# Kernel tuning notes

Hardware: AMD Instinct MI355X
Metric: run time of the kernel (lower is better)

Reference implementation:

```python
import jax, jax.numpy as jnp
import numpy as np

D_MODEL, D_STATE, D_CONV, EXPAND = 1024, 16, 4, 2
D_INNER = EXPAND * D_MODEL
BATCH, L = 2, 2048


def setup_inputs() -> dict:
    key = jax.random.key(0)
    ks = jax.random.split(key, 8)
    s = lambda fan: 1.0 / float(np.sqrt(fan))
    x = jax.random.normal(ks[0], (BATCH, L, D_MODEL), jnp.float32)
    W_in = jax.random.normal(ks[1], (D_MODEL, 2 * D_INNER), jnp.float32) * s(D_MODEL)
    conv_w = jax.random.normal(ks[2], (D_INNER, 1, D_CONV), jnp.float32) * s(D_CONV)
    conv_b = jax.random.normal(ks[3], (D_INNER,), jnp.float32) * 0.1
    W_x = jax.random.normal(ks[4], (D_INNER, 2 * D_STATE + 1), jnp.float32) * s(D_INNER)
    w_dt = jax.random.normal(ks[5], (D_INNER,), jnp.float32)
    b_dt = jax.random.normal(ks[6], (D_INNER,), jnp.float32) * 0.1
    W_out = jax.random.normal(ks[7], (D_INNER, D_MODEL), jnp.float32) * s(D_INNER)
    A_log = jnp.log(jnp.broadcast_to(jnp.arange(1, D_STATE + 1, dtype=jnp.float32), (D_INNER, D_STATE)))
    Dp = jnp.ones((D_INNER,), jnp.float32)
    return dict(x=x, W_in=W_in, conv_w=conv_w, conv_b=conv_b, W_x=W_x,
                w_dt=w_dt, b_dt=b_dt, A_log=A_log, Dp=Dp, W_out=W_out)


def _silu(v):
    return v * jax.nn.sigmoid(v)


def _forward(x, W_in, conv_w, conv_b, W_x, w_dt, b_dt, A_log, Dp, W_out):
    xz = x @ W_in                                   # (B,L,2*Di)
    x_, z = jnp.split(xz, 2, axis=-1)               # (B,L,Di) each
    # causal depthwise conv over length (== torch pad d_conv-1 both sides then [:L])
    xc = jnp.transpose(x_, (0, 2, 1))               # (B,Di,L)
    xc = jax.lax.conv_general_dilated(
        xc, conv_w, window_strides=(1,), padding=[(D_CONV - 1, 0)],
        dimension_numbers=('NCH', 'OIH', 'NCH'), feature_group_count=D_INNER)
    xc = xc + conv_b[None, :, None]
    x_ = _silu(jnp.transpose(xc, (0, 2, 1)))        # (B,L,Di)

    bcd = x_ @ W_x                                  # (B,L,2N+1)
    B_ = bcd[..., :D_STATE]                         # (B,L,N)
    C = bcd[..., D_STATE:2 * D_STATE]               # (B,L,N)
    dt = jax.nn.softplus(bcd[..., -1:] * w_dt + b_dt)  # (B,L,Di)
    A = -jnp.exp(A_log)                             # (Di,N)

    def step(h, inp):
        dt_t, B_t, C_t, x_t = inp                   # (B,Di),(B,N),(B,N),(B,Di)
        dA = jnp.exp(dt_t[..., None] * A)           # (B,Di,N)
        h = dA * h + (dt_t * x_t)[..., None] * B_t[:, None, :]
        y = jnp.einsum('bdn,bn->bd', h, C_t)
        return h, y

    h0 = jnp.zeros((x.shape[0], D_INNER, D_STATE), x.dtype)
    xs = (jnp.transpose(dt, (1, 0, 2)), jnp.transpose(B_, (1, 0, 2)),
          jnp.transpose(C, (1, 0, 2)), jnp.transpose(x_, (1, 0, 2)))
    _, ys = jax.lax.scan(step, h0, xs)              # ys: (L,B,Di)
    y = jnp.transpose(ys, (1, 0, 2)) + x_ * Dp      # skip connection via D
    return (y * _silu(z)) @ W_out                   # (B,L,d_model)


def reference(x, W_in, conv_w, conv_b, W_x, w_dt, b_dt, A_log, Dp, W_out):
    return _forward(x, W_in, conv_w, conv_b, W_x, w_dt, b_dt, A_log, Dp, W_out)
```

## Files before the change

### kernel.cpp

```cpp
#include <hip/hip_runtime.h>
#include <hip/hip_bf16.h>
#include <stdint.h>

#define D_MODEL 1024
#define D_STATE 16
#define D_CONV  4
#define D_INNER 2048
#define BATCH   2
#define SEQLEN  2048
#define NROWS   (BATCH*SEQLEN)
#define BCD_LD  36
#define NCHUNK  64
#define CHUNKLEN (SEQLEN/NCHUNK)
#define KS2     16
#define L2E 1.44269504088896340f

typedef __attribute__((ext_vector_type(8))) short   short8;
typedef __attribute__((ext_vector_type(4))) float   f32x4;

__device__ __forceinline__ uint16_t f2bf(float f) {
    uint32_t u = __float_as_uint(f);
    return (uint16_t)((u + 0x7FFFu + ((u >> 16) & 1u)) >> 16);
}
__device__ __forceinline__ float bf2f(uint16_t h) {
    return __uint_as_float(((uint32_t)h) << 16);
}
__device__ __forceinline__ uint32_t pack2bf(float lo, float hi) {
    return (uint32_t)f2bf(lo) | ((uint32_t)f2bf(hi) << 16);
}
__device__ __forceinline__ void gload16(const uint16_t* g, uint16_t* l) {
    __builtin_amdgcn_global_load_lds(
        (const __attribute__((address_space(1))) void*)g,
        (__attribute__((address_space(3))) void*)l, 16, 0, 0);
}
__device__ __forceinline__ void gload16f(const float* g, float* l) {
    __builtin_amdgcn_global_load_lds(
        (const __attribute__((address_space(1))) void*)g,
        (__attribute__((address_space(3))) void*)l, 16, 0, 0);
}
__device__ __forceinline__ float softplus_f(float v) {
    return fmaxf(v, 0.f) + __logf(1.f + __expf(-fabsf(v)));
}
__device__ __forceinline__ float silu_f(float v) {
    return v / (1.f + __expf(-v));
}
__device__ __forceinline__ short8 pack8(const float4 lo, const float4 hi) {
    short8 r;
    r[0] = (short)f2bf(lo.x); r[1] = (short)f2bf(lo.y);
    r[2] = (short)f2bf(lo.z); r[3] = (short)f2bf(lo.w);
    r[4] = (short)f2bf(hi.x); r[5] = (short)f2bf(hi.y);
    r[6] = (short)f2bf(hi.z); r[7] = (short)f2bf(hi.w);
    return r;
}

__global__ void kcvt(const float* __restrict__ in, uint16_t* __restrict__ out, int n4) {
    int T = blockIdx.x * 256 + threadIdx.x;
    if (T >= n4) return;
    const float4 v = *(const float4*)&in[(size_t)T * 4];
    ushort4 o;
    o.x = f2bf(v.x); o.y = f2bf(v.y); o.z = f2bf(v.z); o.w = f2bf(v.w);
    *(ushort4*)&out[(size_t)T * 4] = o;
}

__global__ void ktrans(const float* __restrict__ in, uint16_t* __restrict__ out,
                       int Kd, int Nd) {
    __shared__ float tile[32][33];
    const int n0 = blockIdx.x * 32, k0 = blockIdx.y * 32;
    const int tx = threadIdx.x & 31, ty = threadIdx.x >> 5;
#pragma unroll
    for (int i = 0; i < 4; ++i)
        tile[ty + i * 8][tx] = in[(size_t)(k0 + ty + i * 8) * Nd + n0 + tx];
    __syncthreads();
#pragma unroll
    for (int i = 0; i < 4; ++i)
        out[(size_t)(n0 + ty + i * 8) * Kd + k0 + tx] = f2bf(tile[tx][ty + i * 8]);
}

__global__ void kwxt(const float* __restrict__ Wx, float* __restrict__ Wxt) {
    const int T = blockIdx.x * 256 + threadIdx.x;
    const int j = T >> 11, k = T & 2047;
    Wxt[T] = (j < 33) ? Wx[(size_t)k * 33 + j] : 0.f;
}

template<int KDIM, int GXL>
__global__ __launch_bounds__(512) void kgemm256(const uint16_t* __restrict__ A,
                                                const uint16_t* __restrict__ B,
                                                uint16_t* __restrict__ C, const int ldc) {
    __shared__ uint16_t As[256 * 32];
    __shared__ uint16_t Bs[128 * 32];
    const int t = threadIdx.x;
    const int w = t >> 6, lane = t & 63;
    int wg = blockIdx.y * (1 << GXL) + blockIdx.x;
    wg = (wg & 7) * ((gridDim.x * gridDim.y) >> 3) + (wg >> 3);
    const int m0 = (wg >> GXL) * 256, n0 = (wg & ((1 << GXL) - 1)) * 128;
    const int wm = (w >> 1) * 64, wn = (w & 1) * 64;
    f32x4 acc[4][4] = {};

    const int srow = t >> 2;
    const int scol = ((t & 3) ^ ((t >> 3) & 3)) * 8;
    const uint16_t* ga0 = A + (size_t)(m0 + srow) * KDIM + scol;
    const uint16_t* ga1 = A + (size_t)(m0 + 128 + srow) * KDIM + scol;
    const uint16_t* gb0 = B + (size_t)(n0 + srow) * KDIM + scol;
    uint16_t* lA0 = &As[w * 512];
    uint16_t* lA1 = &As[4096 + w * 512];
    uint16_t* lB0 = &Bs[w * 512];

    const int fr = lane & 15, fg = (lane >> 4) * 8;
    const int psl = (((fg >> 3) ^ ((fr >> 1) & 3)) << 3);

    for (int kt = 0; kt < KDIM / 32; ++kt) {
        const int ko = kt * 32;
        gload16(ga0 + ko, lA0);
        gload16(ga1 + ko, lA1);
        gload16(gb0 + ko, lB0);
        __syncthreads();
        short8 a[4], b[4];
#pragma unroll
        for (int i = 0; i < 4; ++i) {
            a[i] = *(const short8*)&As[(wm + i * 16 + fr) * 32 + psl];
            b[i] = *(const short8*)&Bs[(wn + i * 16 + fr) * 32 + psl];
        }
#pragma unroll
        for (int i = 0; i < 4; ++i)
#pragma unroll
            for (int j = 0; j < 4; ++j)
                acc[i][j] = __builtin_amdgcn_mfma_f32_16x16x32_bf16(a[i], b[j], acc[i][j], 0, 0, 0);
        __syncthreads();
    }
    const int cr = (lane >> 4) * 4, cc = lane & 15;
#pragma unroll
    for (int i = 0; i < 4; ++i)
#pragma unroll
        for (int j = 0; j < 4; ++j)
#pragma unroll
            for (int r = 0; r < 4; ++r)
                C[(size_t)(m0 + wm + i * 16 + cr + r) * ldc + (n0 + wn + j * 16 + cc)] =
                    f2bf(acc[i][j][r]);
}

template<int KDIM, int GXL>
__global__ __launch_bounds__(256) void kgemm64(const uint16_t* __restrict__ A,
                                               const uint16_t* __restrict__ B,
                                               float* __restrict__ C, const int ldc) {
    __shared__ uint16_t As[64 * 32];
    __shared__ uint16_t Bs[128 * 32];
    const int t = threadIdx.x;
    const int w = t >> 6, lane = t & 63;
    int wg = blockIdx.y * (1 << GXL) + blockIdx.x;
    wg = (wg & 7) * ((gridDim.x * gridDim.y) >> 3) + (wg >> 3);
    const int m0 = (wg >> GXL) * 64, n0 = (wg & ((1 << GXL) - 1)) * 128;
    const int wm = (w >> 1) * 32, wn = (w & 1) * 64;
    f32x4 acc[2][4] = {};

    const int srow = t >> 2;
    const int scol = ((t & 3) ^ ((t >> 3) & 3)) * 8;
    const uint16_t* ga0 = A + (size_t)(m0 + srow) * KDIM + scol;
    const uint16_t* gb0 = B + (size_t)(n0 + srow) * KDIM + scol;
    const uint16_t* gb1 = B + (size_t)(n0 + 64 + srow) * KDIM + scol;
    uint16_t* lA0 = &As[w * 512];
    uint16_t* lB0 = &Bs[w * 512];
    uint16_t* lB1 = &Bs[2048 + w * 512];

    const int fr = lane & 15, fg = (lane >> 4) * 8;
    const int psl = (((fg >> 3) ^ ((fr >> 1) & 3)) << 3);

    for (int kt = 0; kt < KDIM / 32; ++kt) {
        const int ko = kt * 32;
        gload16(ga0 + ko, lA0);
        gload16(gb0 + ko, lB0);
        gload16(gb1 + ko, lB1);
        __syncthreads();
        short8 a[2], b[4];
#pragma unroll
        for (int i = 0; i < 2; ++i)
            a[i] = *(const short8*)&As[(wm + i * 16 + fr) * 32 + psl];
#pragma unroll
        for (int j = 0; j < 4; ++j)
            b[j] = *(const short8*)&Bs[(wn + j * 16 + fr) * 32 + psl];
#pragma unroll
        for (int i = 0; i < 2; ++i)
#pragma unroll
            for (int j = 0; j < 4; ++j)
                acc[i][j] = __builtin_amdgcn_mfma_f32_16x16x32_bf16(a[i], b[j], acc[i][j], 0, 0, 0);
        __syncthreads();
    }
    const int cr = (lane >> 4) * 4, cc = lane & 15;
#pragma unroll
    for (int i = 0; i < 2; ++i)
#pragma unroll
        for (int j = 0; j < 4; ++j)
#pragma unroll
            for (int r = 0; r < 4; ++r)
                C[(size_t)(m0 + wm + i * 16 + cr + r) * ldc + (n0 + wn + j * 16 + cc)] = acc[i][j][r];
}

__global__ __launch_bounds__(256) void kgemm2m(const float* __restrict__ xs,
        const float* __restrict__ Wxt, float* __restrict__ part) {
    __shared__ float As[128 * 32];
    __shared__ float Bs[64 * 32];
    const int t = threadIdx.x;
    const int w = t >> 6, lane = t & 63;
    const int kb = blockIdx.x;
    const int m0 = blockIdx.y * 128;
    const int kc = kb * 128;
    f32x4 acc[2][3] = {};

    const int srow = t >> 3;
    const int scol = ((t & 7) ^ ((t >> 3) & 7)) * 4;
    float* lA[4]; float* lB[2];
#pragma unroll
    for (int r = 0; r < 4; ++r) lA[r] = &As[(r * 32 + w * 8) * 32];
#pragma unroll
    for (int r = 0; r < 2; ++r) lB[r] = &Bs[(r * 32 + w * 8) * 32];

    const int wm = w * 32;
    const int fr = lane & 15, fg = (lane >> 4) * 8;
    const int plo = (((fg >> 2) ^ (fr & 7))) * 4;
    const int phi = ((((fg >> 2) + 1) ^ (fr & 7))) * 4;

    for (int kt = 0; kt < 4; ++kt) {
        const int ko = kc + kt * 32;
#pragma unroll
        for (int r = 0; r < 4; ++r)
            gload16f(xs + (size_t)(m0 + r * 32 + srow) * 2048 + ko + scol, lA[r]);
#pragma unroll
        for (int r = 0; r < 2; ++r)
            gload16f(Wxt + (size_t)(r * 32 + srow) * 2048 + ko + scol, lB[r]);
        __syncthreads();
        short8 a[2], b[3];
#pragma unroll
        for (int i = 0; i < 2; ++i) {
            const float* base = &As[(wm + i * 16 + fr) * 32];
            a[i] = pack8(*(const float4*)&base[plo], *(const float4*)&base[phi]);
        }
#pragma unroll
        for (int j = 0; j < 3; ++j) {
            const float* base = &Bs[(j * 16 + fr) * 32];
            b[j] = pack8(*(const float4*)&base[plo], *(const float4*)&base[phi]);
        }
#pragma unroll
        for (int i = 0; i < 2; ++i)
#pragma unroll
            for (int j = 0; j < 3; ++j)
                acc[i][j] = __builtin_amdgcn_mfma_f32_16x16x32_bf16(a[i], b[j], acc[i][j], 0, 0, 0);
        __syncthreads();
    }
    const int cr = (lane >> 4) * 4, cc = lane & 15;
    float* pb = part + (size_t)kb * 4096 * 48;
#pragma unroll
    for (int i = 0; i < 2; ++i)
#pragma unroll
        for (int j = 0; j < 3; ++j)
#pragma unroll
            for (int r = 0; r < 4; ++r)
                pb[(size_t)(m0 + wm + i * 16 + cr + r) * 48 + j * 16 + cc] = acc[i][j][r];
}

__global__ void kred2(const float* __restrict__ part, float* __restrict__ bcd) {
    const int T = blockIdx.x * 256 + threadIdx.x;
    if (T >= 4096 * 48) return;
    const int row = T / 48, j = T - row * 48;
    if (j >= 33) return;
    float s = 0.f;
#pragma unroll
    for (int ks = 0; ks < KS2; ++ks) s += part[(size_t)ks * 4096 * 48 + T];
    bcd[(size_t)row * BCD_LD + j] = s;
}

__global__ void kprep(const float* __restrict__ bcd, const float* __restrict__ wdt,
                      const float* __restrict__ bdt, const float* __restrict__ Dp,
                      float* __restrict__ xs_io, const uint16_t* __restrict__ xzb,
                      uint32_t* __restrict__ szw) {
    const int T = blockIdx.x * 256 + threadIdx.x;
    const int row = T >> 9, dg = (T & 511) * 4;
    const float raw = bcd[(size_t)row * BCD_LD + 32];
    const float4 w  = *(const float4*)&wdt[dg];
    const float4 b  = *(const float4*)&bdt[dg];
    const float4 Dv = *(const float4*)&Dp[dg];
    const float4 xv = *(const float4*)&xs_io[(size_t)row * 2048 + dg];
    const ushort4 zu = *(const ushort4*)&xzb[(size_t)row * 4096 + 2048 + dg];
    const float dt0 = softplus_f(raw * w.x + b.x);
    const float dt1 = softplus_f(raw * w.y + b.y);
    const float dt2 = softplus_f(raw * w.z + b.z);
    const float dt3 = softplus_f(raw * w.w + b.w);
    float4 pd;
    pd.x = __uint_as_float(pack2bf(dt0, dt0 * xv.x));
    pd.y = __uint_as_float(pack2bf(dt1, dt1 * xv.y));
    pd.z = __uint_as_float(pack2bf(dt2, dt2 * xv.z));
    pd.w = __uint_as_float(pack2bf(dt3, dt3 * xv.w));
    const float s0 = silu_f(bf2f(zu.x)), s1 = silu_f(bf2f(zu.y));
    const float s2 = silu_f(bf2f(zu.z)), s3 = silu_f(bf2f(zu.w));
    uint4 ps;
    ps.x = pack2bf(s0, xv.x * Dv.x * s0);
    ps.y = pack2bf(s1, xv.y * Dv.y * s1);
    ps.z = pack2bf(s2, xv.z * Dv.z * s2);
    ps.w = pack2bf(s3, xv.w * Dv.w * s3);
    *(float4*)&xs_io[(size_t)row * 2048 + dg] = pd;
    *(uint4*)&szw[(size_t)row * 2048 + dg] = ps;
}

__global__ __launch_bounds__(256) void kscan1(const uint32_t* __restrict__ dtdx,
        const float* __restrict__ bcd, const float* __restrict__ Alog,
        float* __restrict__ hbuf, float* __restrict__ sumdt) {
    const int T = blockIdx.x * 256 + threadIdx.x;
    const int sub = T & 1;
    const int cp  = (T >> 1) & 2047;
    const int chunk = T >> 12;
    const int b = cp >> 10, d0 = (cp & 1023) * 2;
    float Ae0[8], Ae1[8]; bool st = true;
#pragma unroll
    for (int i = 0; i < 8; ++i) {
        const float a0 = __expf(Alog[d0 * 16 + sub * 8 + i]);
        const float a1 = __expf(Alog[(d0 + 1) * 16 + sub * 8 + i]);
        Ae0[i] = -a0 * L2E; Ae1[i] = -a1 * L2E;
        st = st && (fabsf(a0 - (float)(sub * 8 + i + 1)) < 1e-3f)
                && (fabsf(a1 - (float)(sub * 8 + i + 1)) < 1e-3f);
    }
    float hA[8] = {}, hB[8] = {};
    float sdtA = 0.f, sdtB = 0.f;
    const int row0 = b * SEQLEN + chunk * CHUNKLEN;
    const uint32_t* pD = dtdx + (size_t)row0 * 2048 + d0;
    const float* pB = bcd + (size_t)row0 * BCD_LD + sub * 8;
    if (st) {
        for (int l0 = 0; l0 < CHUNKLEN; l0 += 2) {
            uint2 pk[2]; float4 B0[2], B1[2];
#pragma unroll
            for (int s = 0; s < 2; ++s) {
                pk[s] = *(const uint2*)(pD + (size_t)s * 2048);
                B0[s] = *(const float4*)(pB + s * BCD_LD);
                B1[s] = *(const float4*)(pB + s * BCD_LD + 4);
            }
#pragma unroll
            for (int s = 0; s < 2; ++s) {
                const float dtA  = __uint_as_float(pk[s].x << 16);
                const float dtxA = __uint_as_float(pk[s].x & 0xffff0000u);
                const float dtB  = __uint_as_float(pk[s].y << 16);
                const float dtxB = __uint_as_float(pk[s].y & 0xffff0000u);
                sdtA += dtA; sdtB += dtB;
                const float e0A = __builtin_amdgcn_exp2f(dtA * (-L2E));
                const float e0B = __builtin_amdgcn_exp2f(dtB * (-L2E));
                const float e8A = (e0A*e0A)*(e0A*e0A)*(e0A*e0A)*(e0A*e0A);
                const float e8B = (e0B*e0B)*(e0B*e0B)*(e0B*e0B)*(e0B*e0B);
                float dA = sub ? e8A : 1.f, dB = sub ? e8B : 1.f;
                dA *= e0A; dB *= e0B; hA[0] = fmaf(dA, hA[0], dtxA * B0[s].x); hB[0] = fmaf(dB, hB[0], dtxB * B0[s].x);
                dA *= e0A; dB *= e0B; hA[1] = fmaf(dA, hA[1], dtxA * B0[s].y); hB[1] = fmaf(dB, hB[1], dtxB * B0[s].y);
                dA *= e0A; dB *= e0B; hA[2] = fmaf(dA, hA[2], dtxA * B0[s].z); hB[2] = fmaf(dB, hB[2], dtxB * B0[s].z);
                dA *= e0A; dB *= e0B; hA[3] = fmaf(dA, hA[3], dtxA * B0[s].w); hB[3] = fmaf(dB, hB[3], dtxB * B0[s].w);
                dA *= e0A; dB *= e0B; hA[4] = fmaf(dA, hA[4], dtxA * B1[s].x); hB[4] = fmaf(dB, hB[4], dtxB * B1[s].x);
                dA *= e0A; dB *= e0B; hA[5] = fmaf(dA, hA[5], dtxA * B1[s].y); hB[5] = fmaf(dB, hB[5], dtxB * B1[s].y);
                dA *= e0A; dB *= e0B; hA[6] = fmaf(dA, hA[6], dtxA * B1[s].z); hB[6] = fmaf(dB, hB[6], dtxB * B1[s].z);
                dA *= e0A; dB *= e0B; hA[7] = fmaf(dA, hA[7], dtxA * B1[s].w); hB[7] = fmaf(dB, hB[7], dtxB * B1[s].w);
            }
            pD += 2 * 2048; pB += 2 * BCD_LD;
        }
    } else {
        for (int l0 = 0; l0 < CHUNKLEN; l0 += 2) {
            uint2 pk[2]; float4 B0[2], B1[2];
#pragma unroll
            for (int s = 0; s < 2; ++s) {
                pk[s] = *(const uint2*)(pD + (size_t)s * 2048);
                B0[s] = *(const float4*)(pB + s * BCD_LD);
                B1[s] = *(const float4*)(pB + s * BCD_LD + 4);
            }
#pragma unroll
            for (int s = 0; s < 2; ++s) {
                const float dtA  = __uint_as_float(pk[s].x << 16);
                const float dtxA = __uint_as_float(pk[s].x & 0xffff0000u);
                const float dtB  = __uint_as_float(pk[s].y << 16);
                const float dtxB = __uint_as_float(pk[s].y & 0xffff0000u);
                sdtA += dtA; sdtB += dtB;
                const float Bv[8] = {B0[s].x, B0[s].y, B0[s].z, B0[s].w,
                                     B1[s].x, B1[s].y, B1[s].z, B1[s].w};
#pragma unroll
                for (int i = 0; i < 8; ++i) {
                    hA[i] = fmaf(__builtin_amdgcn_exp2f(dtA * Ae0[i]), hA[i], dtxA * Bv[i]);
                    hB[i] = fmaf(__builtin_amdgcn_exp2f(dtB * Ae1[i]), hB[i], dtxB * Bv[i]);
                }
            }
            pD += 2 * 2048; pB += 2 * BCD_LD;
        }
    }
    const size_t cc0 = (size_t)(chunk * 4096 + b * 2048 + d0) * 16 + sub * 8;
    *(float4*)&hbuf[cc0]          = make_float4(hA[0], hA[1], hA[2], hA[3]);
    *(float4*)&hbuf[cc0 + 4]      = make_float4(hA[4], hA[5], hA[6], hA[7]);
    *(float4*)&hbuf[cc0 + 16]     = make_float4(hB[0], hB[1], hB[2], hB[3]);
    *(float4*)&hbuf[cc0 + 20]     = make_float4(hB[4], hB[5], hB[6], hB[7]);
    if (sub == 0)
        *(float2*)&sumdt[chunk * 4096 + b * 2048 + d0] = make_float2(sdtA, sdtB);
}

__global__ void kscan2(float* __restrict__ hbuf, const float* __restrict__ sumdt,
                       const float* __restrict__ Alog) {
    const int T = blockIdx.x * 256 + threadIdx.x;
    const int n = T & 15, ch = T >> 4;
    const int d = ch & 2047;
    const float Ae = -__expf(Alog[d * 16 + n]) * L2E;
    float h = 0.f;
    for (int c = 0; c < NCHUNK; ++c) {
        const size_t idx = (size_t)(c * 4096 + ch) * 16 + n;
        const float loc = hbuf[idx];
        hbuf[idx] = h;
        h = __builtin_amdgcn_exp2f(Ae * sumdt[c * 4096 + ch]) * h + loc;
    }
}

__global__ __launch_bounds__(256) void kscan3(const uint32_t* __restrict__ dtdx,
        const float* __restrict__ bcd, const float* __restrict__ Alog,
        const uint32_t* __restrict__ szw, const float* __restrict__ hbuf,
        uint16_t* __restrict__ u) {
    const int T = blockIdx.x * 256 + threadIdx.x;
    const int sub = T & 1;
    const int cp  = (T >> 1) & 2047;
    const int chunk = T >> 12;
    const int b = cp >> 10, d0 = (cp & 1023) * 2;
    float Ae0[8], Ae1[8]; bool st = true;
#pragma unroll
    for (int i = 0; i < 8; ++i) {
        const float a0 = __expf(Alog[d0 * 16 + sub * 8 + i]);
        const float a1 = __expf(Alog[(d0 + 1) * 16 + sub * 8 + i]);
        Ae0[i] = -a0 * L2E; Ae1[i] = -a1 * L2E;
        st = st && (fabsf(a0 - (float)(sub * 8 + i + 1)) < 1e-3f)
                && (fabsf(a1 - (float)(sub * 8 + i + 1)) < 1e-3f);
    }
    float hA[8], hB[8];
    {
        const size_t cc0 = (size_t)(chunk * 4096 + b * 2048 + d0) * 16 + sub * 8;
        const float4 a0 = *(const float4*)&hbuf[cc0];
        const float4 a1 = *(const float4*)&hbuf[cc0 + 4];
        const float4 b0 = *(const float4*)&hbuf[cc0 + 16];
        const float4 b1 = *(const float4*)&hbuf[cc0 + 20];
        hA[0]=a0.x; hA[1]=a0.y; hA[2]=a0.z; hA[3]=a0.w;
        hA[4]=a1.x; hA[5]=a1.y; hA[6]=a1.z; hA[7]=a1.w;
        hB[0]=b0.x; hB[1]=b0.y; hB[2]=b0.z; hB[3]=b0.w;
        hB[4]=b1.x; hB[5]=b1.y; hB[6]=b1.z; hB[7]=b1.w;
    }
    const int row0 = b * SEQLEN + chunk * CHUNKLEN;
    const uint32_t* pD = dtdx + (size_t)row0 * 2048 + d0;
    const uint32_t* pS = szw  + (size_t)row0 * 2048 + d0;
    const float* pB = bcd + (size_t)row0 * BCD_LD + sub * 8;
    uint16_t* pU = u + (size_t)row0 * D_INNER + d0;
    if (st) {
        for (int l0 = 0; l0 < CHUNKLEN; l0 += 2) {
            uint2 pk[2], qk[2]; float4 B0[2], B1[2], C0[2], C1[2];
#pragma unroll
            for (int s = 0; s < 2; ++s) {
                pk[s] = *(const uint2*)(pD + (size_t)s * 2048);
                B0[s] = *(const float4*)(pB + s * BCD_LD);
                B1[s] = *(const float4*)(pB + s * BCD_LD + 4);
                C0[s] = *(const float4*)(pB + s * BCD_LD + 16);
                C1[s] = *(const float4*)(pB + s * BCD_LD + 20);
                if (sub == 0) qk[s] = *(const uint2*)(pS + (size_t)s * 2048);
            }
#pragma unroll
            for (int s = 0; s < 2; ++s) {
                const float dtA  = __uint_as_float(pk[s].x << 16);
                const float dtxA = __uint_as_float(pk[s].x & 0xffff0000u);
                const float dtB  = __uint_as_float(pk[s].y << 16);
                const float dtxB = __uint_as_float(pk[s].y & 0xffff0000u);
                const float e0A = __builtin_amdgcn_exp2f(dtA * (-L2E));
                const float e0B = __builtin_amdgcn_exp2f(dtB * (-L2E));
                const float e8A = (e0A*e0A)*(e0A*e0A)*(e0A*e0A)*(e0A*e0A);
                const float e8B = (e0B*e0B)*(e0B*e0B)*(e0B*e0B)*(e0B*e0B);
                float dA = sub ? e8A : 1.f, dB = sub ? e8B : 1.f;
                float yA, yB;
                dA *= e0A; dB *= e0B; hA[0] = fmaf(dA, hA[0], dtxA * B0[s].x); hB[0] = fmaf(dB, hB[0], dtxB * B0[s].x);
                dA *= e0A; dB *= e0B; hA[1] = fmaf(dA, hA[1], dtxA * B0[s].y); hB[1] = fmaf(dB, hB[1], dtxB * B0[s].y);
                dA *= e0A; dB *= e0B; hA[2] = fmaf(dA, hA[2], dtxA * B0[s].z); hB[2] = fmaf(dB, hB[2], dtxB * B0[s].z);
                dA *= e0A; dB *= e0B; hA[3] = fmaf(dA, hA[3], dtxA * B0[s].w); hB[3] = fmaf(dB, hB[3], dtxB * B0[s].w);
                dA *= e0A; dB *= e0B; hA[4] = fmaf(dA, hA[4], dtxA * B1[s].x); hB[4] = fmaf(dB, hB[4], dtxB * B1[s].x);
                dA *= e0A; dB *= e0B; hA[5] = fmaf(dA, hA[5], dtxA * B1[s].y); hB[5] = fmaf(dB, hB[5], dtxB * B1[s].y);
                dA *= e0A; dB *= e0B; hA[6] = fmaf(dA, hA[6], dtxA * B1[s].z); hB[6] = fmaf(dB, hB[6], dtxB * B1[s].z);
                dA *= e0A; dB *= e0B; hA[7] = fmaf(dA, hA[7], dtxA * B1[s].w); hB[7] = fmaf(dB, hB[7], dtxB * B1[s].w);
                yA = hA[0]*C0[s].x + hA[1]*C0[s].y + hA[2]*C0[s].z + hA[3]*C0[s].w
                   + hA[4]*C1[s].x + hA[5]*C1[s].y + hA[6]*C1[s].z + hA[7]*C1[s].w;
                yB = hB[0]*C0[s].x + hB[1]*C0[s].y + hB[2]*C0[s].z + hB[3]*C0[s].w
                   + hB[4]*C1[s].x + hB[5]*C1[s].y + hB[6]*C1[s].z + hB[7]*C1[s].w;
                yA += __shfl_xor(yA, 1);
                yB += __shfl_xor(yB, 1);
                if (sub == 0) {
                    const float szA = __uint_as_float(qk[s].x << 16);
                    const float w2A = __uint_as_float(qk[s].x & 0xffff0000u);
                    const float szB = __uint_as_float(qk[s].y << 16);
                    const float w2B = __uint_as_float(qk[s].y & 0xffff0000u);
                    *(uint32_t*)(pU + (size_t)s * D_INNER) =
                        pack2bf(fmaf(yA, szA, w2A), fmaf(yB, szB, w2B));
                }
            }
            pD += 2 * 2048; pS += 2 * 2048; pB += 2 * BCD_LD; pU += 2 * D_INNER;
        }
    } else {
        for (int l0 = 0; l0 < CHUNKLEN; l0 += 2) {
            uint2 pk[2], qk[2]; float4 B0[2], B1[2], C0[2], C1[2];
#pragma unroll
            for (int s = 0; s < 2; ++s) {
                pk[s] = *(const uint2*)(pD + (size_t)s * 2048);
                B0[s] = *(const float4*)(pB + s * BCD_LD);
                B1[s] = *(const float4*)(pB + s * BCD_LD + 4);
                C0[s] = *(const float4*)(pB + s * BCD_LD + 16);
                C1[s] = *(const float4*)(pB + s * BCD_LD + 20);
                if (sub == 0) qk[s] = *(const uint2*)(pS + (size_t)s * 2048);
            }
#pragma unroll
            for (int s = 0; s < 2; ++s) {
                const float dtA  = __uint_as_float(pk[s].x << 16);
                const float dtxA = __uint_as_float(pk[s].x & 0xffff0000u);
                const float dtB  = __uint_as_float(pk[s].y << 16);
                const float dtxB = __uint_as_float(pk[s].y & 0xffff0000u);
                const float Bv[8] = {B0[s].x, B0[s].y, B0[s].z, B0[s].w,
                                     B1[s].x, B1[s].y, B1[s].z, B1[s].w};
                const float Cv[8] = {C0[s].x, C0[s].y, C0[s].z, C0[s].w,
                                     C1[s].x, C1[s].y, C1[s].z, C1[s].w};
                float yA = 0.f, yB = 0.f;
#pragma unroll
                for (int i = 0; i < 8; ++i) {
                    hA[i] = fmaf(__builtin_amdgcn_exp2f(dtA * Ae0[i]), hA[i], dtxA * Bv[i]);
                    hB[i] = fmaf(__builtin_amdgcn_exp2f(dtB * Ae1[i]), hB[i], dtxB * Bv[i]);
                    yA = fmaf(hA[i], Cv[i], yA);
                    yB = fmaf(hB[i], Cv[i], yB);
                }
                yA += __shfl_xor(yA, 1);
                yB += __shfl_xor(yB, 1);
                if (sub == 0) {
                    const float szA = __uint_as_float(qk[s].x << 16);
                    const float w2A = __uint_as_float(qk[s].x & 0xffff0000u);
                    const float szB = __uint_as_float(qk[s].y << 16);
                    const float w2B = __uint_as_float(qk[s].y & 0xffff0000u);
                    *(uint32_t*)(pU + (size_t)s * D_INNER) =
                        pack2bf(fmaf(yA, szA, w2A), fmaf(yB, szB, w2B));
                }
            }
            pD += 2 * 2048; pS += 2 * 2048; pB += 2 * BCD_LD; pU += 2 * D_INNER;
        }
    }
}

__global__ void kconv(const uint16_t* __restrict__ xzb, const float* __restrict__ cw,
                      const float* __restrict__ cb, float* __restrict__ xs) {
    const int T = blockIdx.x * 256 + threadIdx.x;
    const int d0 = (T & 1023) * 2;
    const int row = T >> 10;
    const int l = row & (SEQLEN - 1), b = row >> 11;
    const float4 wA = *(const float4*)&cw[d0 * 4];
    const float4 wB = *(const float4*)&cw[d0 * 4 + 4];
    const float2 bias = *(const float2*)&cb[d0];
    float a0 = bias.x, a1 = bias.y;
    const size_t base = (size_t)b * SEQLEN;
    if (l >= 3) {
        uint32_t v;
        v = *(const uint32_t*)&xzb[(base + l - 3) * 4096 + d0];
        a0 += wA.x * bf2f((uint16_t)v); a1 += wB.x * bf2f((uint16_t)(v >> 16));
        v = *(const uint32_t*)&xzb[(base + l - 2) * 4096 + d0];
        a0 += wA.y * bf2f((uint16_t)v); a1 += wB.y * bf2f((uint16_t)(v >> 16));
        v = *(const uint32_t*)&xzb[(base + l - 1) * 4096 + d0];
        a0 += wA.z * bf2f((uint16_t)v); a1 += wB.z * bf2f((uint16_t)(v >> 16));
        v = *(const uint32_t*)&xzb[(base + l    ) * 4096 + d0];
        a0 += wA.w * bf2f((uint16_t)v); a1 += wB.w * bf2f((uint16_t)(v >> 16));
    } else {
        uint32_t v;
        if (l >= 2) {
            v = *(const uint32_t*)&xzb[(base + l - 2) * 4096 + d0];
            a0 += wA.y * bf2f((uint16_t)v); a1 += wB.y * bf2f((uint16_t)(v >> 16));
        }
        if (l >= 1) {
            v = *(const uint32_t*)&xzb[(base + l - 1) * 4096 + d0];
            a0 += wA.z * bf2f((uint16_t)v); a1 += wB.z * bf2f((uint16_t)(v >> 16));
        }
        v = *(const uint32_t*)&xzb[(base + l) * 4096 + d0];
        a0 += wA.w * bf2f((uint16_t)v); a1 += wB.w * bf2f((uint16_t)(v >> 16));
    }
    *(float2*)&xs[(size_t)row * 2048 + d0] = make_float2(silu_f(a0), silu_f(a1));
}

extern "C" void kernel_launch(void* const* d_in, const int* in_sizes, int n_in,
                              void* d_out, int out_size, void* d_ws, size_t ws_size,
                              hipStream_t stream) {
    const float* x      = (const float*)d_in[0];
    const float* W_in   = (const float*)d_in[1];
    const float* conv_w = (const float*)d_in[2];
    const float* conv_b = (const float*)d_in[3];
    const float* W_x    = (const float*)d_in[4];
    const float* w_dt   = (const float*)d_in[5];
    const float* b_dt   = (const float*)d_in[6];
    const float* A_log  = (const float*)d_in[7];
    const float* Dp     = (const float*)d_in[8];
    const float* W_out  = (const float*)d_in[9];
    float* out = (float*)d_out;

    char* p = (char*)d_ws;
    uint16_t* xb  = (uint16_t*)p;  p += (size_t)NROWS * D_MODEL * 2;
    uint16_t* Wb  = (uint16_t*)p;  p += (size_t)4096 * 1024 * 2;
    uint16_t* Wob = (uint16_t*)p;  p += (size_t)1024 * 2048 * 2;
    uint16_t* xzb = (uint16_t*)p;  p += (size_t)NROWS * 4096 * 2;
    float* xs     = (float*)p;     p += (size_t)NROWS * D_INNER * 4;
    float* bcd    = (float*)p;     p += (size_t)NROWS * BCD_LD * 4;
    float* sumdt  = (float*)p;     p += (size_t)NCHUNK * 4096 * 4;
    float* Wxt    = (float*)p;     p += (size_t)64 * 2048 * 4;
    uint16_t* ub  = (uint16_t*)p;  p += (size_t)NROWS * D_INNER * 2;
    uint32_t* szw = (uint32_t*)p;  p += (size_t)NROWS * D_INNER * 4;
    float* hbuf   = (float*)xb;
    float* part   = (float*)ub;
    uint32_t* dtdx = (uint32_t*)xs;

    kcvt<<<(NROWS * D_MODEL / 4 + 255) / 256, 256, 0, stream>>>(x, xb, NROWS * D_MODEL / 4);
    ktrans<<<dim3(4096 / 32, 1024 / 32), 256, 0, stream>>>(W_in, Wb, 1024, 4096);
    ktrans<<<dim3(1024 / 32, 2048 / 32), 256, 0, stream>>>(W_out, Wob, 2048, 1024);
    kwxt<<<(64 * 2048) / 256, 256, 0, stream>>>(W_x, Wxt);
    kgemm256<1024, 5><<<dim3(32, 16), 512, 0, stream>>>(xb, Wb, xzb, 4096);
    kconv<<<NROWS * 1024 / 256, 256, 0, stream>>>(xzb, conv_w, conv_b, xs);
    kgemm2m<<<dim3(KS2, 32), 256, 0, stream>>>(xs, Wxt, part);
    kred2<<<(4096 * 48 + 255) / 256, 256, 0, stream>>>(part, bcd);
    kprep<<<(4096 * 512) / 256, 256, 0, stream>>>(bcd, w_dt, b_dt, Dp, xs, xzb, szw);
    kscan1<<<(4096 * NCHUNK) / 256, 256, 0, stream>>>(dtdx, bcd, A_log, hbuf, sumdt);
    kscan2<<<(4096 * 16) / 256, 256, 0, stream>>>(hbuf, sumdt, A_log);
    kscan3<<<(4096 * NCHUNK) / 256, 256, 0, stream>>>(dtdx, bcd, A_log, szw, hbuf, ub);
    kgemm64<2048, 3><<<dim3(1024 / 128, 4096 / 64), 256, 0, stream>>>(ub, Wob, out, 1024);
}
```

Measured before the change: 222.2 us.

## Double-buffer GEMM LDS tiles and stage scan B/C rows in shared memory

Both bf16 MFMA GEMM kernels now keep two LDS buffers and issue the next K-tile's global loads before computing on the current one. This removes one barrier per iteration and overlaps load latency with MFMA work, at the cost of doubled LDS use and possibly lower occupancy. The two scan kernels also preload the chunk's B/C rows from bcd into shared memory once per block instead of re-reading them from global memory every step. The shared load assumes each block covers exactly one chunk and batch, which the thread indexing appears to satisfy.

```diff
diff --git a/kernel.cpp b/kernel.cpp
--- a/kernel.cpp
+++ b/kernel.cpp
@@ -86,8 +86,8 @@
 __global__ __launch_bounds__(512) void kgemm256(const uint16_t* __restrict__ A,
                                                 const uint16_t* __restrict__ B,
                                                 uint16_t* __restrict__ C, const int ldc) {
-    __shared__ uint16_t As[256 * 32];
-    __shared__ uint16_t Bs[128 * 32];
+    __shared__ uint16_t As[2][256 * 32];
+    __shared__ uint16_t Bsh[2][128 * 32];
     const int t = threadIdx.x;
     const int w = t >> 6, lane = t & 63;
     int wg = blockIdx.y * (1 << GXL) + blockIdx.x;
@@ -101,24 +101,26 @@
     const uint16_t* ga0 = A + (size_t)(m0 + srow) * KDIM + scol;
     const uint16_t* ga1 = A + (size_t)(m0 + 128 + srow) * KDIM + scol;
     const uint16_t* gb0 = B + (size_t)(n0 + srow) * KDIM + scol;
-    uint16_t* lA0 = &As[w * 512];
-    uint16_t* lA1 = &As[4096 + w * 512];
-    uint16_t* lB0 = &Bs[w * 512];
 
     const int fr = lane & 15, fg = (lane >> 4) * 8;
     const int psl = (((fg >> 3) ^ ((fr >> 1) & 3)) << 3);
 
+    auto stage = [&](int buf, int ko) {
+        gload16(ga0 + ko, &As[buf][w * 512]);
+        gload16(ga1 + ko, &As[buf][4096 + w * 512]);
+        gload16(gb0 + ko, &Bsh[buf][w * 512]);
+    };
+
+    stage(0, 0);
+    __syncthreads();
+    int cur = 0;
     for (int kt = 0; kt < KDIM / 32; ++kt) {
-        const int ko = kt * 32;
-        gload16(ga0 + ko, lA0);
-        gload16(ga1 + ko, lA1);
-        gload16(gb0 + ko, lB0);
-        __syncthreads();
+        if (kt + 1 < KDIM / 32) stage(cur ^ 1, (kt + 1) * 32);
         short8 a[4], b[4];
 #pragma unroll
         for (int i = 0; i < 4; ++i) {
-            a[i] = *(const short8*)&As[(wm + i * 16 + fr) * 32 + psl];
-            b[i] = *(const short8*)&Bs[(wn + i * 16 + fr) * 32 + psl];
+            a[i] = *(const short8*)&As[cur][(wm + i * 16 + fr) * 32 + psl];
+            b[i] = *(const short8*)&Bsh[cur][(wn + i * 16 + fr) * 32 + psl];
         }
 #pragma unroll
         for (int i = 0; i < 4; ++i)
@@ -126,6 +128,7 @@
             for (int j = 0; j < 4; ++j)
                 acc[i][j] = __builtin_amdgcn_mfma_f32_16x16x32_bf16(a[i], b[j], acc[i][j], 0, 0, 0);
         __syncthreads();
+        cur ^= 1;
     }
     const int cr = (lane >> 4) * 4, cc = lane & 15;
 #pragma unroll
@@ -142,8 +145,8 @@
 __global__ __launch_bounds__(256) void kgemm64(const uint16_t* __restrict__ A,
                                                const uint16_t* __restrict__ B,
                                                float* __restrict__ C, const int ldc) {
-    __shared__ uint16_t As[64 * 32];
-    __shared__ uint16_t Bs[128 * 32];
+    __shared__ uint16_t As[2][64 * 32];
+    __shared__ uint16_t Bsh[2][128 * 32];
     const int t = threadIdx.x;
     const int w = t >> 6, lane = t & 63;
     int wg = blockIdx.y * (1 << GXL) + blockIdx.x;
@@ -157,32 +160,35 @@
     const uint16_t* ga0 = A + (size_t)(m0 + srow) * KDIM + scol;
     const uint16_t* gb0 = B + (size_t)(n0 + srow) * KDIM + scol;
     const uint16_t* gb1 = B + (size_t)(n0 + 64 + srow) * KDIM + scol;
-    uint16_t* lA0 = &As[w * 512];
-    uint16_t* lB0 = &Bs[w * 512];
-    uint16_t* lB1 = &Bs[2048 + w * 512];
 
     const int fr = lane & 15, fg = (lane >> 4) * 8;
     const int psl = (((fg >> 3) ^ ((fr >> 1) & 3)) << 3);
 
+    auto stage = [&](int buf, int ko) {
+        gload16(ga0 + ko, &As[buf][w * 512]);
+        gload16(gb0 + ko, &Bsh[buf][w * 512]);
+        gload16(gb1 + ko, &Bsh[buf][2048 + w * 512]);
+    };
+
+    stage(0, 0);
+    __syncthreads();
+    int cur = 0;
     for (int kt = 0; kt < KDIM / 32; ++kt) {
-        const int ko = kt * 32;
-        gload16(ga0 + ko, lA0);
-        gload16(gb0 + ko, lB0);
-        gload16(gb1 + ko, lB1);
-        __syncthreads();
+        if (kt + 1 < KDIM / 32) stage(cur ^ 1, (kt + 1) * 32);
         short8 a[2], b[4];
 #pragma unroll
         for (int i = 0; i < 2; ++i)
-            a[i] = *(const short8*)&As[(wm + i * 16 + fr) * 32 + psl];
+            a[i] = *(const short8*)&As[cur][(wm + i * 16 + fr) * 32 + psl];
 #pragma unroll
         for (int j = 0; j < 4; ++j)
-            b[j] = *(const short8*)&Bs[(wn + j * 16 + fr) * 32 + psl];
+            b[j] = *(const short8*)&Bsh[cur][(wn + j * 16 + fr) * 32 + psl];
 #pragma unroll
         for (int i = 0; i < 2; ++i)
 #pragma unroll
             for (int j = 0; j < 4; ++j)
                 acc[i][j] = __builtin_amdgcn_mfma_f32_16x16x32_bf16(a[i], b[j], acc[i][j], 0, 0, 0);
         __syncthreads();
+        cur ^= 1;
     }
     const int cr = (lane >> 4) * 4, cc = lane & 15;
 #pragma unroll
@@ -307,6 +313,16 @@
     const int cp  = (T >> 1) & 2047;
     const int chunk = T >> 12;
     const int b = cp >> 10, d0 = (cp & 1023) * 2;
+    const int row0 = b * SEQLEN + chunk * CHUNKLEN;
+
+    __shared__ float Bls[32][16];
+    {
+        const int r = threadIdx.x >> 3, c = (threadIdx.x & 7) * 2;
+        const float2 v = *(const float2*)&bcd[(size_t)(row0 + r) * BCD_LD + c];
+        Bls[r][c] = v.x; Bls[r][c + 1] = v.y;
+    }
+    __syncthreads();
+
     float Ae0[8], Ae1[8]; bool st = true;
 #pragma unroll
     for (int i = 0; i < 8; ++i) {
@@ -318,17 +334,15 @@
     }
     float hA[8] = {}, hB[8] = {};
     float sdtA = 0.f, sdtB = 0.f;
-    const int row0 = b * SEQLEN + chunk * CHUNKLEN;
     const uint32_t* pD = dtdx + (size_t)row0 * 2048 + d0;
-    const float* pB = bcd + (size_t)row0 * BCD_LD + sub * 8;
     if (st) {
         for (int l0 = 0; l0 < CHUNKLEN; l0 += 2) {
             uint2 pk[2]; float4 B0[2], B1[2];
 #pragma unroll
             for (int s = 0; s < 2; ++s) {
                 pk[s] = *(const uint2*)(pD + (size_t)s * 2048);
-                B0[s] = *(const float4*)(pB + s * BCD_LD);
-                B1[s] = *(const float4*)(pB + s * BCD_LD + 4);
+                B0[s] = *(const float4*)&Bls[l0 + s][sub * 8];
+                B1[s] = *(const float4*)&Bls[l0 + s][sub * 8 + 4];
             }
 #pragma unroll
             for (int s = 0; s < 2; ++s) {
@@ -351,7 +365,7 @@
                 dA *= e0A; dB *= e0B; hA[6] = fmaf(dA, hA[6], dtxA * B1[s].z); hB[6] = fmaf(dB, hB[6], dtxB * B1[s].z);
                 dA *= e0A; dB *= e0B; hA[7] = fmaf(dA, hA[7], dtxA * B1[s].w); hB[7] = fmaf(dB, hB[7], dtxB * B1[s].w);
             }
-            pD += 2 * 2048; pB += 2 * BCD_LD;
+            pD += 2 * 2048;
         }
     } else {
         for (int l0 = 0; l0 < CHUNKLEN; l0 += 2) {
@@ -359,8 +373,8 @@
 #pragma unroll
             for (int s = 0; s < 2; ++s) {
                 pk[s] = *(const uint2*)(pD + (size_t)s * 2048);
-                B0[s] = *(const float4*)(pB + s * BCD_LD);
-                B1[s] = *(const float4*)(pB + s * BCD_LD + 4);
+                B0[s] = *(const float4*)&Bls[l0 + s][sub * 8];
+                B1[s] = *(const float4*)&Bls[l0 + s][sub * 8 + 4];
             }
 #pragma unroll
             for (int s = 0; s < 2; ++s) {
@@ -377,7 +391,7 @@
                     hB[i] = fmaf(__builtin_amdgcn_exp2f(dtB * Ae1[i]), hB[i], dtxB * Bv[i]);
                 }
             }
-            pD += 2 * 2048; pB += 2 * BCD_LD;
+            pD += 2 * 2048;
         }
     }
     const size_t cc0 = (size_t)(chunk * 4096 + b * 2048 + d0) * 16 + sub * 8;
@@ -413,6 +427,15 @@
     const int cp  = (T >> 1) & 2047;
     const int chunk = T >> 12;
     const int b = cp >> 10, d0 = (cp & 1023) * 2;
+    const int row0 = b * SEQLEN + chunk * CHUNKLEN;
+
+    __shared__ float BC[32][32];
+    {
+        const int r = threadIdx.x >> 3, c = (threadIdx.x & 7) * 4;
+        *(float4*)&BC[r][c] = *(const float4*)&bcd[(size_t)(row0 + r) * BCD_LD + c];
+    }
+    __syncthreads();
+
     float Ae0[8], Ae1[8]; bool st = true;
 #pragma unroll
     for (int i = 0; i < 8; ++i) {
@@ -434,10 +457,8 @@
         hB[0]=b0.x; hB[1]=b0.y; hB[2]=b0.z; hB[3]=b0.w;
         hB[4]=b1.x; hB[5]=b1.y; hB[6]=b1.z; hB[7]=b1.w;
     }
-    const int row0 = b * SEQLEN + chunk * CHUNKLEN;
     const uint32_t* pD = dtdx + (size_t)row0 * 2048 + d0;
     const uint32_t* pS = szw  + (size_t)row0 * 2048 + d0;
-    const float* pB = bcd + (size_t)row0 * BCD_LD + sub * 8;
     uint16_t* pU = u + (size_t)row0 * D_INNER + d0;
     if (st) {
         for (int l0 = 0; l0 < CHUNKLEN; l0 += 2) {
@@ -445,10 +466,10 @@
 #pragma unroll
             for (int s = 0; s < 2; ++s) {
                 pk[s] = *(const uint2*)(pD + (size_t)s * 2048);
-                B0[s] = *(const float4*)(pB + s * BCD_LD);
-                B1[s] = *(const float4*)(pB + s * BCD_LD + 4);
-                C0[s] = *(const float4*)(pB + s * BCD_LD + 16);
-                C1[s] = *(const float4*)(pB + s * BCD_LD + 20);
+                B0[s] = *(const float4*)&BC[l0 + s][sub * 8];
+                B1[s] = *(const float4*)&BC[l0 + s][sub * 8 + 4];
+                C0[s] = *(const float4*)&BC[l0 + s][16 + sub * 8];
+                C1[s] = *(const float4*)&BC[l0 + s][20 + sub * 8];
                 if (sub == 0) qk[s] = *(const uint2*)(pS + (size_t)s * 2048);
             }
 #pragma unroll
@@ -486,7 +507,7 @@
                         pack2bf(fmaf(yA, szA, w2A), fmaf(yB, szB, w2B));
                 }
             }
-            pD += 2 * 2048; pS += 2 * 2048; pB += 2 * BCD_LD; pU += 2 * D_INNER;
+            pD += 2 * 2048; pS += 2 * 2048; pU += 2 * D_INNER;
         }
     } else {
         for (int l0 = 0; l0 < CHUNKLEN; l0 += 2) {
@@ -494,10 +515,10 @@
 #pragma unroll
             for (int s = 0; s < 2; ++s) {
                 pk[s] = *(const uint2*)(pD + (size_t)s * 2048);
-                B0[s] = *(const float4*)(pB + s * BCD_LD);
-                B1[s] = *(const float4*)(pB + s * BCD_LD + 4);
-                C0[s] = *(const float4*)(pB + s * BCD_LD + 16);
-                C1[s] = *(const float4*)(pB + s * BCD_LD + 20);
+                B0[s] = *(const float4*)&BC[l0 + s][sub * 8];
+                B1[s] = *(const float4*)&BC[l0 + s][sub * 8 + 4];
+                C0[s] = *(const float4*)&BC[l0 + s][16 + sub * 8];
+                C1[s] = *(const float4*)&BC[l0 + s][20 + sub * 8];
                 if (sub == 0) qk[s] = *(const uint2*)(pS + (size_t)s * 2048);
             }
 #pragma unroll
@@ -529,7 +550,7 @@
                         pack2bf(fmaf(yA, szA, w2A), fmaf(yB, szB, w2B));
                 }
             }
-            pD += 2 * 2048; pS += 2 * 2048; pB += 2 * BCD_LD; pU += 2 * D_INNER;
+            pD += 2 * 2048; pS += 2 * 2048; pU += 2 * D_INNER;
         }
     }
 }
```

Measured after the change: 221.3 us. No clear change (-0.4%).
